# Kernel tuning notes

Measured on AMD Instinct MI355X. Metric: run time of the kernel, lower is better.

Reference implementation:

```python
import jax, jax.numpy as jnp
import numpy as np

N_LAYERS = 3

def setup_inputs() -> dict:
    key = jax.random.key(0)
    k1, k2, k3, k4, k5 = jax.random.split(key, 5)
    num_users, num_items, d = 100000, 200000, 64
    N = num_users + num_items
    nnz = 5000000
    user_emb = jax.random.normal(k1, (num_users, d), dtype=jnp.float32) * 0.1
    item_emb = jax.random.normal(k2, (num_items, d), dtype=jnp.float32) * 0.1
    adj_rows = jax.random.randint(k3, (nnz,), 0, N, dtype=jnp.int32)
    adj_cols = jax.random.randint(k4, (nnz,), 0, N, dtype=jnp.int32)
    # normalized-adjacency-like values (positive, O(1/deg) scale)
    adj_vals = jax.random.uniform(k5, (nnz,), dtype=jnp.float32) / 16.0
    return {"user_emb": user_emb, "item_emb": item_emb, "adj_vals": adj_vals,
            "adj_rows": adj_rows, "adj_cols": adj_cols}

def reference(user_emb, item_emb, adj_vals, adj_rows, adj_cols):
    num_users = user_emb.shape[0]
    N = num_users + item_emb.shape[0]
    ego = jnp.concatenate([user_emb, item_emb], axis=0)  # [N, D]
    acc = jnp.zeros_like(ego)
    for _ in range(N_LAYERS):
        # SpMM: out[r] += vals[e] * ego[cols[e]] for each edge e with row r
        msgs = adj_vals[:, None] * ego[adj_cols]          # [nnz, D]
        ego = jax.ops.segment_sum(msgs, adj_rows, num_segments=N)
        acc = acc + ego                                   # fused running-mean accumulator
    mean_emb = acc / N_LAYERS
    return mean_emb[:num_users], mean_emb[num_users:]
```

## Files before the change

kernel.cpp:

```cpp
#include <hip/hip_runtime.h>

constexpr int GS_BLOCKS = 2048;
constexpr int THREADS   = 256;
constexpr int RB_LOG    = 9;
constexpr int RB        = 1 << RB_LOG;
constexpr int CH        = 8192;
constexpr int BT_BIN    = 1024;
constexpr int COL_BITS  = 19;
constexpr int COL_MASK  = (1 << COL_BITS) - 1;
constexpr int MAX_NB    = 1024;
constexpr int BH_BLOCKS = 1024;

typedef _Float16 h4 __attribute__((ext_vector_type(4)));
typedef int      i4 __attribute__((ext_vector_type(4)));

__global__ void k_tofp16(const float4* __restrict__ u, const float4* __restrict__ it,
                         h4* __restrict__ dst, int uf4, int tot) {
  int stride = gridDim.x * blockDim.x;
  for (int i = blockIdx.x * blockDim.x + threadIdx.x; i < tot; i += stride) {
    float4 v = (i < uf4) ? u[i] : it[i - uf4];
    h4 o;
    o[0] = (_Float16)v.x; o[1] = (_Float16)v.y;
    o[2] = (_Float16)v.z; o[3] = (_Float16)v.w;
    dst[i] = o;
  }
}

__global__ void k_concat(const float4* __restrict__ u, const float4* __restrict__ it,
                         float4* __restrict__ dst, int uf4, int tot) {
  int stride = gridDim.x * blockDim.x;
  for (int i = blockIdx.x * blockDim.x + threadIdx.x; i < tot; i += stride)
    dst[i] = (i < uf4) ? u[i] : it[i - uf4];
}

__global__ void k_bhist(const int* __restrict__ rows, int nnz, int nB,
                        int* __restrict__ bucket_cnt) {
  __shared__ int lcnt[MAX_NB];
  int t = threadIdx.x;
  for (int j = t; j < nB; j += THREADS) lcnt[j] = 0;
  __syncthreads();
  int gid = blockIdx.x * blockDim.x + t;
  int stride = gridDim.x * blockDim.x;
  int nnz4 = nnz >> 2;
  const i4* r4 = (const i4*)rows;
  for (int i = gid; i < nnz4; i += stride) {
    i4 v = __builtin_nontemporal_load(r4 + i);
    atomicAdd(&lcnt[v[0] >> RB_LOG], 1);
    atomicAdd(&lcnt[v[1] >> RB_LOG], 1);
    atomicAdd(&lcnt[v[2] >> RB_LOG], 1);
    atomicAdd(&lcnt[v[3] >> RB_LOG], 1);
  }
  for (int i = (nnz4 << 2) + gid; i < nnz; i += stride)
    atomicAdd(&lcnt[__builtin_nontemporal_load(rows + i) >> RB_LOG], 1);
  __syncthreads();
  for (int j = t; j < nB; j += THREADS)
    if (lcnt[j]) atomicAdd(&bucket_cnt[j], lcnt[j]);
}

__global__ void __launch_bounds__(1024)
k_scan_buckets(const int* __restrict__ bucket_cnt, int nB,
               int* __restrict__ bucket_base, int* __restrict__ bucket_fill) {
  __shared__ int a[1024];
  int t = threadIdx.x;
  int mine = (t < nB) ? bucket_cnt[t] : 0;
  a[t] = mine; __syncthreads();
  for (int off = 1; off < 1024; off <<= 1) {
    int x = (t >= off) ? a[t - off] : 0;
    __syncthreads();
    a[t] += x;
    __syncthreads();
  }
  int excl = a[t] - mine;
  if (t < nB) { bucket_base[t] = excl; bucket_fill[t] = excl; }
  if (t == 1023) bucket_base[nB] = a[1023];
}

__global__ void __launch_bounds__(BT_BIN)
k_bin(const int* __restrict__ rows, const int* __restrict__ cols,
      const float* __restrict__ vals, int nnz, int nB,
      int* __restrict__ bucket_fill, int2* __restrict__ binned) {
  __shared__ int bcnt[MAX_NB];
  __shared__ int bfill[MAX_NB];
  __shared__ int rstash[CH];
  int t = threadIdx.x;
  int c0 = blockIdx.x * CH;
  if (t < nB) { bcnt[t] = 0; bfill[t] = 0; }
  __syncthreads();
#pragma unroll
  for (int k = 0; k < CH / BT_BIN; k++) {
    int e = c0 + t + k * BT_BIN;
    if (e < nnz) {
      int r = __builtin_nontemporal_load(rows + e);
      rstash[t + k * BT_BIN] = r;
      atomicAdd(&bcnt[r >> RB_LOG], 1);
    }
  }
  __syncthreads();
  if (t < nB) {
    int c = bcnt[t];
    bcnt[t] = (c > 0) ? atomicAdd(&bucket_fill[t], c) : 0;
  }
  __syncthreads();
#pragma unroll
  for (int k = 0; k < CH / BT_BIN; k++) {
    int e = c0 + t + k * BT_BIN;
    if (e < nnz) {
      int r = rstash[t + k * BT_BIN];
      int b = r >> RB_LOG;
      int rank = atomicAdd(&bfill[b], 1);
      int packed = ((r & (RB - 1)) << COL_BITS) | __builtin_nontemporal_load(cols + e);
      binned[bcnt[b] + rank] =
          make_int2(packed, __float_as_int(__builtin_nontemporal_load(vals + e)));
    }
  }
}

__global__ void __launch_bounds__(1024)
k_bucket_sedge(const int2* __restrict__ binned, const int* __restrict__ bucket_base,
               int* __restrict__ row_ptr, int N, int nnz, int2* __restrict__ sedge) {
  __shared__ int rcnt[RB];
  __shared__ int sarr[RB];
  int b = blockIdx.x, t = threadIdx.x;
  int e0 = bucket_base[b], e1 = bucket_base[b + 1];
  if (t < RB) rcnt[t] = 0;
  __syncthreads();
  for (int j = e0 + t; j < e1; j += 1024)
    atomicAdd(&rcnt[(unsigned)binned[j].x >> COL_BITS], 1);
  __syncthreads();
  int mine = (t < RB) ? rcnt[t] : 0;
  if (t < RB) sarr[t] = mine;
  __syncthreads();
  for (int off = 1; off < RB; off <<= 1) {
    int x = 0;
    if (t < RB && t >= off) x = sarr[t - off];
    __syncthreads();
    if (t < RB) sarr[t] += x;
    __syncthreads();
  }
  if (t < RB) {
    int excl = sarr[t] - mine;
    int grow = (b << RB_LOG) + t;
    if (grow < N) row_ptr[grow] = e0 + excl;
    rcnt[t] = e0 + excl;
  }
  if (b == 0 && t == 0) row_ptr[N] = nnz;
  __syncthreads();
  for (int j = e0 + t; j < e1; j += 1024) {
    int2 ed = binned[j];
    int rL = (unsigned)ed.x >> COL_BITS;
    int pos = atomicAdd(&rcnt[rL], 1);
    sedge[pos] = make_int2(ed.x & COL_MASK, ed.y);
  }
}

__global__ void __launch_bounds__(THREADS)
k_spmm_h(const int* __restrict__ row_ptr, const int2* __restrict__ sedge,
         const _Float16* __restrict__ prev, _Float16* __restrict__ next,
         float* __restrict__ out, int n, int layer) {
  int gid = blockIdx.x * blockDim.x + threadIdx.x;
  int row = gid >> 4, l = gid & 15;
  if (row >= n) return;
  int s = row_ptr[row], e = row_ptr[row + 1];
  float ax = 0.f, ay = 0.f, az = 0.f, aw = 0.f;
  float bx = 0.f, by = 0.f, bz = 0.f, bw = 0.f;
  auto gat = [&](int c) -> h4 {
    return *reinterpret_cast<const h4*>(prev + (size_t)c * 64 + l * 4);
  };
  int j = s;
  if (j < e && (j & 1)) {
    int2 ed = sedge[j];
    float v = __int_as_float(ed.y);
    h4 g = gat(ed.x);
    ax = fmaf(v, (float)g[0], ax); ay = fmaf(v, (float)g[1], ay);
    az = fmaf(v, (float)g[2], az); aw = fmaf(v, (float)g[3], aw);
    ++j;
  }
  for (; j + 4 <= e; j += 4) {
    int4 e01 = *reinterpret_cast<const int4*>(sedge + j);
    int4 e23 = *reinterpret_cast<const int4*>(sedge + j + 2);
    h4 g0 = gat(e01.x), g1 = gat(e01.z), g2 = gat(e23.x), g3 = gat(e23.z);
    float v0 = __int_as_float(e01.y), v1 = __int_as_float(e01.w);
    float v2 = __int_as_float(e23.y), v3 = __int_as_float(e23.w);
    ax = fmaf(v0, (float)g0[0], ax); ay = fmaf(v0, (float)g0[1], ay);
    az = fmaf(v0, (float)g0[2], az); aw = fmaf(v0, (float)g0[3], aw);
    bx = fmaf(v1, (float)g1[0], bx); by = fmaf(v1, (float)g1[1], by);
    bz = fmaf(v1, (float)g1[2], bz); bw = fmaf(v1, (float)g1[3], bw);
    ax = fmaf(v2, (float)g2[0], ax); ay = fmaf(v2, (float)g2[1], ay);
    az = fmaf(v2, (float)g2[2], az); aw = fmaf(v2, (float)g2[3], aw);
    bx = fmaf(v3, (float)g3[0], bx); by = fmaf(v3, (float)g3[1], by);
    bz = fmaf(v3, (float)g3[2], bz); bw = fmaf(v3, (float)g3[3], bw);
  }
  if (j + 2 <= e) {
    int4 e01 = *reinterpret_cast<const int4*>(sedge + j);
    h4 g0 = gat(e01.x), g1 = gat(e01.z);
    float v0 = __int_as_float(e01.y), v1 = __int_as_float(e01.w);
    ax = fmaf(v0, (float)g0[0], ax); ay = fmaf(v0, (float)g0[1], ay);
    az = fmaf(v0, (float)g0[2], az); aw = fmaf(v0, (float)g0[3], aw);
    bx = fmaf(v1, (float)g1[0], bx); by = fmaf(v1, (float)g1[1], by);
    bz = fmaf(v1, (float)g1[2], bz); bw = fmaf(v1, (float)g1[3], bw);
    j += 2;
  }
  if (j < e) {
    int2 ed = sedge[j];
    float v = __int_as_float(ed.y);
    h4 g = gat(ed.x);
    ax = fmaf(v, (float)g[0], ax); ay = fmaf(v, (float)g[1], ay);
    az = fmaf(v, (float)g[2], az); aw = fmaf(v, (float)g[3], aw);
  }
  ax += bx; ay += by; az += bz; aw += bw;
  if (layer != 2) {
    h4 o;
    o[0] = (_Float16)ax; o[1] = (_Float16)ay;
    o[2] = (_Float16)az; o[3] = (_Float16)aw;
    *reinterpret_cast<h4*>(next + (size_t)row * 64 + l * 4) = o;
  }
  float4* op = reinterpret_cast<float4*>(out + (size_t)row * 64 + l * 4);
  if (layer == 0) {
    *op = make_float4(ax, ay, az, aw);
  } else if (layer == 1) {
    float4 o = *op; o.x += ax; o.y += ay; o.z += az; o.w += aw; *op = o;
  } else {
    const float inv3 = 1.0f / 3.0f;
    float4 o = *op;
    o.x = (o.x + ax) * inv3; o.y = (o.y + ay) * inv3;
    o.z = (o.z + az) * inv3; o.w = (o.w + aw) * inv3;
    *op = o;
  }
}

__global__ void k_edge_atomic(const int* __restrict__ rows, const int* __restrict__ cols,
                              const float* __restrict__ vals, long long tot16,
                              const float* __restrict__ prev, float* __restrict__ nxt) {
  long long stride = (long long)gridDim.x * blockDim.x;
  for (long long i = (long long)blockIdx.x * blockDim.x + threadIdx.x; i < tot16; i += stride) {
    int e = (int)(i >> 4), l = (int)(i & 15);
    int r = rows[e], c = cols[e];
    float v = vals[e];
    const float4 x = *reinterpret_cast<const float4*>(prev + (size_t)c * 64 + l * 4);
    float* d = nxt + (size_t)r * 64 + l * 4;
    atomicAdd(d + 0, v * x.x); atomicAdd(d + 1, v * x.y);
    atomicAdd(d + 2, v * x.z); atomicAdd(d + 3, v * x.w);
  }
}

__global__ void k_accum(const float4* __restrict__ nxt, float4* __restrict__ out, int tot, int layer) {
  int stride = gridDim.x * blockDim.x;
  for (int i = blockIdx.x * blockDim.x + threadIdx.x; i < tot; i += stride) {
    float4 a = nxt[i];
    if (layer == 0) {
      out[i] = a;
    } else if (layer == 1) {
      float4 o = out[i]; o.x += a.x; o.y += a.y; o.z += a.z; o.w += a.w; out[i] = o;
    } else {
      const float inv3 = 1.0f / 3.0f;
      float4 o = out[i];
      o.x = (o.x + a.x) * inv3; o.y = (o.y + a.y) * inv3;
      o.z = (o.z + a.z) * inv3; o.w = (o.w + a.w) * inv3;
      out[i] = o;
    }
  }
}

extern "C" void kernel_launch(void* const* d_in, const int* in_sizes, int n_in,
                              void* d_out, int out_size, void* d_ws, size_t ws_size,
                              hipStream_t stream) {
  const float* user = (const float*)d_in[0];
  const float* item = (const float*)d_in[1];
  const float* vals = (const float*)d_in[2];
  const int*   rows = (const int*)d_in[3];
  const int*   cols = (const int*)d_in[4];
  const int D = 64;
  const int num_users = in_sizes[0] / D;
  const int num_items = in_sizes[1] / D;
  const int nnz = in_sizes[2];
  const int N = num_users + num_items;
  float* out = (float*)d_out;

  size_t off = 0;
  auto carve = [&](size_t bytes) -> char* {
    char* p = (char*)d_ws + off;
    off = (off + bytes + 255) & ~(size_t)255;
    return p;
  };
  size_t egoBytesF = (size_t)N * D * sizeof(float);
  size_t egoBytesH = (size_t)N * D * sizeof(_Float16);
  char* region1 = carve(egoBytesF);
  char* region2 = carve(egoBytesF);
  int nB = (N + RB - 1) >> RB_LOG;
  int*  row_ptr     = (int*)carve((size_t)(N + 1) * 4);
  int*  bucket_cnt  = (int*)carve((size_t)nB * 4);
  int*  bucket_base = (int*)carve((size_t)(nB + 1) * 4);
  int*  bucket_fill = (int*)carve((size_t)nB * 4);
  int2* sedge       = (int2*)carve((size_t)nnz * 8);

  _Float16* egoA_h = (_Float16*)region1;
  _Float16* egoB_h = (_Float16*)(region1 + egoBytesH);
  int2*     binned = (int2*)region2;
  bool use_csr = (off <= ws_size) && (nB <= MAX_NB) &&
                 ((size_t)nnz * 8 <= egoBytesF) && (N < (1 << COL_BITS)) &&
                 (2 * egoBytesH <= egoBytesF);

  if (use_csr) {
    hipMemsetAsync(bucket_cnt, 0, (size_t)nB * 4, stream);
    k_bhist<<<BH_BLOCKS, THREADS, 0, stream>>>(rows, nnz, nB, bucket_cnt);
    k_scan_buckets<<<1, 1024, 0, stream>>>(bucket_cnt, nB, bucket_base, bucket_fill);
    int nchunks = (nnz + CH - 1) / CH;
    k_bin<<<nchunks, BT_BIN, 0, stream>>>(rows, cols, vals, nnz, nB, bucket_fill, binned);
    k_bucket_sedge<<<nB, 1024, 0, stream>>>(binned, bucket_base, row_ptr, N, nnz, sedge);
    int totF4 = N * (D / 4);
    int uf4   = num_users * (D / 4);
    k_tofp16<<<GS_BLOCKS, THREADS, 0, stream>>>((const float4*)user, (const float4*)item,
                                                (h4*)egoA_h, uf4, totF4);

    int spmm_blocks = (N * 16 + THREADS - 1) / THREADS;
    k_spmm_h<<<spmm_blocks, THREADS, 0, stream>>>(row_ptr, sedge, egoA_h, egoB_h, out, N, 0);
    k_spmm_h<<<spmm_blocks, THREADS, 0, stream>>>(row_ptr, sedge, egoB_h, egoA_h, out, N, 1);
    k_spmm_h<<<spmm_blocks, THREADS, 0, stream>>>(row_ptr, sedge, egoA_h, egoB_h, out, N, 2);
  } else {
    float* egoA = (float*)region1;
    float* egoB = (float*)region2;
    int totF4 = N * (D / 4);
    int uf4   = num_users * (D / 4);
    k_concat<<<GS_BLOCKS, THREADS, 0, stream>>>((const float4*)user, (const float4*)item,
                                                (float4*)egoA, uf4, totF4);
    float* prev = egoA;
    float* next = egoB;
    long long tot16 = (long long)nnz * 16;
    for (int layer = 0; layer < 3; ++layer) {
      hipMemsetAsync(next, 0, egoBytesF, stream);
      k_edge_atomic<<<GS_BLOCKS * 2, THREADS, 0, stream>>>(rows, cols, vals, tot16, prev, next);
      k_accum<<<GS_BLOCKS, THREADS, 0, stream>>>((const float4*)next, (float4*)out, totF4, layer);
      float* t = prev; prev = next; next = t;
    }
  }
}
```

Before: 535.0 us.

## Widen SpMM gathers to 8 halfs and defer layer averaging to merge kernel

SpMM now assigns 8 lanes per row with 16-byte fp16 gathers and writes only fp16 layer outputs into three rotating buffers (reusing the binned-edge region). A separate merge kernel averages the three fp16 layers into the fp32 output, replacing per-layer fp32 read-modify-write traffic on the output. This cuts output memory traffic and gather instruction count, but the final layer is now rounded to fp16 before averaging, slightly reducing precision.

```diff
diff --git a/kernel.cpp b/kernel.cpp
--- a/kernel.cpp
+++ b/kernel.cpp
@@ -12,6 +12,8 @@
 constexpr int BH_BLOCKS = 1024;
 
 typedef _Float16 h4 __attribute__((ext_vector_type(4)));
+typedef _Float16 h8 __attribute__((ext_vector_type(8)));
+typedef float    f8 __attribute__((ext_vector_type(8)));
 typedef int      i4 __attribute__((ext_vector_type(4)));
 
 __global__ void k_tofp16(const float4* __restrict__ u, const float4* __restrict__ it,
@@ -154,77 +156,60 @@
 }
 
 __global__ void __launch_bounds__(THREADS)
-k_spmm_h(const int* __restrict__ row_ptr, const int2* __restrict__ sedge,
-         const _Float16* __restrict__ prev, _Float16* __restrict__ next,
-         float* __restrict__ out, int n, int layer) {
+k_spmm_h8(const int* __restrict__ row_ptr, const int2* __restrict__ sedge,
+          const _Float16* __restrict__ prev, _Float16* __restrict__ next, int n) {
   int gid = blockIdx.x * blockDim.x + threadIdx.x;
-  int row = gid >> 4, l = gid & 15;
+  int row = gid >> 3, l = gid & 7;
   if (row >= n) return;
   int s = row_ptr[row], e = row_ptr[row + 1];
-  float ax = 0.f, ay = 0.f, az = 0.f, aw = 0.f;
-  float bx = 0.f, by = 0.f, bz = 0.f, bw = 0.f;
-  auto gat = [&](int c) -> h4 {
-    return *reinterpret_cast<const h4*>(prev + (size_t)c * 64 + l * 4);
+  f8 acc = 0.f, accb = 0.f;
+  auto gat = [&](int c) -> f8 {
+    h8 g = *reinterpret_cast<const h8*>(prev + (size_t)c * 64 + l * 8);
+    return __builtin_convertvector(g, f8);
   };
   int j = s;
   if (j < e && (j & 1)) {
     int2 ed = sedge[j];
-    float v = __int_as_float(ed.y);
-    h4 g = gat(ed.x);
-    ax = fmaf(v, (float)g[0], ax); ay = fmaf(v, (float)g[1], ay);
-    az = fmaf(v, (float)g[2], az); aw = fmaf(v, (float)g[3], aw);
+    acc += __int_as_float(ed.y) * gat(ed.x);
     ++j;
   }
   for (; j + 4 <= e; j += 4) {
     int4 e01 = *reinterpret_cast<const int4*>(sedge + j);
     int4 e23 = *reinterpret_cast<const int4*>(sedge + j + 2);
-    h4 g0 = gat(e01.x), g1 = gat(e01.z), g2 = gat(e23.x), g3 = gat(e23.z);
-    float v0 = __int_as_float(e01.y), v1 = __int_as_float(e01.w);
-    float v2 = __int_as_float(e23.y), v3 = __int_as_float(e23.w);
-    ax = fmaf(v0, (float)g0[0], ax); ay = fmaf(v0, (float)g0[1], ay);
-    az = fmaf(v0, (float)g0[2], az); aw = fmaf(v0, (float)g0[3], aw);
-    bx = fmaf(v1, (float)g1[0], bx); by = fmaf(v1, (float)g1[1], by);
-    bz = fmaf(v1, (float)g1[2], bz); bw = fmaf(v1, (float)g1[3], bw);
-    ax = fmaf(v2, (float)g2[0], ax); ay = fmaf(v2, (float)g2[1], ay);
-    az = fmaf(v2, (float)g2[2], az); aw = fmaf(v2, (float)g2[3], aw);
-    bx = fmaf(v3, (float)g3[0], bx); by = fmaf(v3, (float)g3[1], by);
-    bz = fmaf(v3, (float)g3[2], bz); bw = fmaf(v3, (float)g3[3], bw);
+    f8 g0 = gat(e01.x), g1 = gat(e01.z), g2 = gat(e23.x), g3 = gat(e23.z);
+    acc  += __int_as_float(e01.y) * g0;
+    accb += __int_as_float(e01.w) * g1;
+    acc  += __int_as_float(e23.y) * g2;
+    accb += __int_as_float(e23.w) * g3;
   }
   if (j + 2 <= e) {
     int4 e01 = *reinterpret_cast<const int4*>(sedge + j);
-    h4 g0 = gat(e01.x), g1 = gat(e01.z);
-    float v0 = __int_as_float(e01.y), v1 = __int_as_float(e01.w);
-    ax = fmaf(v0, (float)g0[0], ax); ay = fmaf(v0, (float)g0[1], ay);
-    az = fmaf(v0, (float)g0[2], az); aw = fmaf(v0, (float)g0[3], aw);
-    bx = fmaf(v1, (float)g1[0], bx); by = fmaf(v1, (float)g1[1], by);
-    bz = fmaf(v1, (float)g1[2], bz); bw = fmaf(v1, (float)g1[3], bw);
+    f8 g0 = gat(e01.x), g1 = gat(e01.z);
+    acc  += __int_as_float(e01.y) * g0;
+    accb += __int_as_float(e01.w) * g1;
     j += 2;
   }
   if (j < e) {
     int2 ed = sedge[j];
-    float v = __int_as_float(ed.y);
-    h4 g = gat(ed.x);
-    ax = fmaf(v, (float)g[0], ax); ay = fmaf(v, (float)g[1], ay);
-    az = fmaf(v, (float)g[2], az); aw = fmaf(v, (float)g[3], aw);
-  }
-  ax += bx; ay += by; az += bz; aw += bw;
-  if (layer != 2) {
-    h4 o;
-    o[0] = (_Float16)ax; o[1] = (_Float16)ay;
-    o[2] = (_Float16)az; o[3] = (_Float16)aw;
-    *reinterpret_cast<h4*>(next + (size_t)row * 64 + l * 4) = o;
-  }
-  float4* op = reinterpret_cast<float4*>(out + (size_t)row * 64 + l * 4);
-  if (layer == 0) {
-    *op = make_float4(ax, ay, az, aw);
-  } else if (layer == 1) {
-    float4 o = *op; o.x += ax; o.y += ay; o.z += az; o.w += aw; *op = o;
-  } else {
-    const float inv3 = 1.0f / 3.0f;
-    float4 o = *op;
-    o.x = (o.x + ax) * inv3; o.y = (o.y + ay) * inv3;
-    o.z = (o.z + az) * inv3; o.w = (o.w + aw) * inv3;
-    *op = o;
+    acc += __int_as_float(ed.y) * gat(ed.x);
+  }
+  acc += accb;
+  *reinterpret_cast<h8*>(next + (size_t)row * 64 + l * 8) =
+      __builtin_convertvector(acc, h8);
+}
+
+__global__ void k_merge(const h8* __restrict__ A, const h8* __restrict__ B,
+                        const h8* __restrict__ C, float* __restrict__ out, int tot8) {
+  int stride = gridDim.x * blockDim.x;
+  const f8 inv3 = 1.0f / 3.0f;
+  for (int i = blockIdx.x * blockDim.x + threadIdx.x; i < tot8; i += stride) {
+    f8 s = (__builtin_convertvector(A[i], f8) +
+            __builtin_convertvector(B[i], f8) +
+            __builtin_convertvector(C[i], f8)) * inv3;
+    float4 lo = make_float4(s[0], s[1], s[2], s[3]);
+    float4 hi = make_float4(s[4], s[5], s[6], s[7]);
+    float4* op = reinterpret_cast<float4*>(out + (size_t)i * 8);
+    op[0] = lo; op[1] = hi;
   }
 }
 
@@ -295,6 +280,7 @@
 
   _Float16* egoA_h = (_Float16*)region1;
   _Float16* egoB_h = (_Float16*)(region1 + egoBytesH);
+  _Float16* egoC_h = (_Float16*)region2;
   int2*     binned = (int2*)region2;
   bool use_csr = (off <= ws_size) && (nB <= MAX_NB) &&
                  ((size_t)nnz * 8 <= egoBytesF) && (N < (1 << COL_BITS)) &&
@@ -312,10 +298,13 @@
     k_tofp16<<<GS_BLOCKS, THREADS, 0, stream>>>((const float4*)user, (const float4*)item,
                                                 (h4*)egoA_h, uf4, totF4);
 
-    int spmm_blocks = (N * 16 + THREADS - 1) / THREADS;
-    k_spmm_h<<<spmm_blocks, THREADS, 0, stream>>>(row_ptr, sedge, egoA_h, egoB_h, out, N, 0);
-    k_spmm_h<<<spmm_blocks, THREADS, 0, stream>>>(row_ptr, sedge, egoB_h, egoA_h, out, N, 1);
-    k_spmm_h<<<spmm_blocks, THREADS, 0, stream>>>(row_ptr, sedge, egoA_h, egoB_h, out, N, 2);
+    int spmm_blocks = (N * 8 + THREADS - 1) / THREADS;
+    k_spmm_h8<<<spmm_blocks, THREADS, 0, stream>>>(row_ptr, sedge, egoA_h, egoB_h, N);
+    k_spmm_h8<<<spmm_blocks, THREADS, 0, stream>>>(row_ptr, sedge, egoB_h, egoC_h, N);
+    k_spmm_h8<<<spmm_blocks, THREADS, 0, stream>>>(row_ptr, sedge, egoC_h, egoA_h, N);
+    int tot8 = N * (D / 8);
+    k_merge<<<GS_BLOCKS, THREADS, 0, stream>>>((const h8*)egoB_h, (const h8*)egoC_h,
+                                               (const h8*)egoA_h, out, tot8);
   } else {
     float* egoA = (float*)region1;
     float* egoB = (float*)region2;
```

Result: no change. 527.1 us (-1.5%).
